# Performance work log

Hardware: AMD Instinct MI355X
Metric: run time of the kernel (lower is better)

Reference implementation:

```python
import jax, jax.numpy as jnp
import numpy as np

TEMPERATURE = 8.0  # sqrt(head_dim=64)
NEG_FILL = -1000000000.0

def setup_inputs() -> dict:
    key = jax.random.key(0)
    k1, k2, k3, k4, k5 = jax.random.split(key, 5)
    B, H, S, D = 4, 16, 1024, 64
    q = jax.random.normal(k1, (B, H, S, D), dtype=jnp.float32)
    k = jax.random.normal(k2, (B, H, S, D), dtype=jnp.float32)
    v = jax.random.normal(k3, (B, H, S, D), dtype=jnp.float32)
    similarity = jax.random.normal(k4, (B, H, S, S), dtype=jnp.float32)
    mask = jax.random.randint(k5, (B, 1, S, S), 0, 2).astype(bool)
    return {"q": q, "k": k, "v": v, "similarity": similarity, "mask": mask}

def reference(q, k, v, similarity, mask):
    # scores: [B,H,S,S] = (q/temp) @ k^T
    attn = jnp.einsum('bhqd,bhkd->bhqk', q / TEMPERATURE, k)
    attn = jnp.where(mask, NEG_FILL, attn)          # masked_fill (mask broadcasts over heads)
    attn = jax.nn.softmax(attn + similarity, axis=-1)  # dropout p=0 (eval): identity
    output = jnp.einsum('bhqk,bhkd->bhqd', attn, v)
    return (output, attn)
```

## Files before the change

kernel.cpp:

```cpp
#include <hip/hip_runtime.h>
#include <stdint.h>


#define S_LEN 1024
#define D_DIM 64
#define QT 16
#define SSTR 1032
#define NEG_FILL (-1000000000.0f)
#define LOG2E 1.44269504088896340736f

typedef __bf16 bf16x8 __attribute__((ext_vector_type(8)));
typedef float f32x4 __attribute__((ext_vector_type(4)));
typedef unsigned short u16x4 __attribute__((ext_vector_type(4)));
typedef unsigned short u16x8 __attribute__((ext_vector_type(8)));

__device__ __forceinline__ unsigned short f2bf(float x) {
    unsigned u = __builtin_bit_cast(unsigned, x);
    u += 0x7fffu + ((u >> 16) & 1u);
    return (unsigned short)(u >> 16);
}
__device__ __forceinline__ float bf2f(unsigned short b) {
    return __builtin_bit_cast(float, (unsigned)b << 16);
}

__global__ void prep_qkm(const float* __restrict__ q, const float* __restrict__ k,
                         const void* __restrict__ mraw,
                         unsigned short* __restrict__ Qb, unsigned short* __restrict__ Kb,
                         unsigned char* __restrict__ Mb)
{
    const int t = threadIdx.x;
    const int i = blockIdx.x * 256 + t;
    f32x4 q4 = ((const f32x4*)q)[i];
    f32x4 k4 = ((const f32x4*)k)[i];
    u16x4 qo, ko;
#pragma unroll
    for (int j = 0; j < 4; ++j) {
        qo[j] = f2bf(q4[j] * 0.125f);
        ko[j] = f2bf(k4[j]);
    }
    ((u16x4*)Qb)[i] = qo;
    ((u16x4*)Kb)[i] = ko;

    __shared__ int s_not_int, s_not_f32;
    if (t == 0) { s_not_int = 0; s_not_f32 = 0; }
    __syncthreads();
    const unsigned* wdd = (const unsigned*)mraw;
    int ni = 0, nf = 0;
    for (int j = t; j < 1024; j += 256) {
        unsigned x = wdd[j];
        if (x > 1u) ni = 1;
        if (x != 0u && x != 0x3f800000u) nf = 1;
    }
    if (ni) s_not_int = 1;
    if (nf) s_not_f32 = 1;
    __syncthreads();
    const int fmt = (s_not_int == 0) ? 0 : ((s_not_f32 == 0) ? 1 : 2);
    uchar4 o;
    if (fmt == 0) {
        int4 x = ((const int4*)mraw)[i];
        o.x = x.x ? 1 : 0; o.y = x.y ? 1 : 0; o.z = x.z ? 1 : 0; o.w = x.w ? 1 : 0;
    } else if (fmt == 1) {
        float4 x = ((const float4*)mraw)[i];
        o.x = (x.x != 0.f) ? 1 : 0; o.y = (x.y != 0.f) ? 1 : 0;
        o.z = (x.z != 0.f) ? 1 : 0; o.w = (x.w != 0.f) ? 1 : 0;
    } else {
        uchar4 x = ((const uchar4*)mraw)[i];
        o.x = x.x ? 1 : 0; o.y = x.y ? 1 : 0; o.z = x.z ? 1 : 0; o.w = x.w ? 1 : 0;
    }
    ((uchar4*)Mb)[i] = o;
}

__global__ void prep_vt(const float* __restrict__ v, unsigned short* __restrict__ Vt)
{
    __shared__ unsigned short sT[64 * 72];
    const int bh = blockIdx.x >> 4;
    const int st = blockIdx.x & 15;
    const int t = threadIdx.x;
    const float* vb = v + (size_t)(bh * S_LEN + st * 64) * D_DIM;
#pragma unroll
    for (int p = 0; p < 4; ++p) {
        int lin = p * 256 + t;
        int r = lin >> 4;
        int c = lin & 15;
        f32x4 x = ((const f32x4*)(vb + r * D_DIM))[c];
        unsigned short* dst = &sT[r * 72 + c * 4];
#pragma unroll
        for (int j = 0; j < 4; ++j) dst[j] = f2bf(x[j]);
    }
    __syncthreads();
    unsigned short* ob = Vt + (size_t)bh * D_DIM * S_LEN + st * 64;
#pragma unroll
    for (int p = 0; p < 4; ++p) {
        int lin = p * 256 + t;
        int d = lin >> 4;
        int s4 = (lin & 15) * 4;
        u16x4 o;
#pragma unroll
        for (int j = 0; j < 4; ++j) o[j] = sT[(s4 + j) * 72 + d];
        *(u16x4*)&ob[d * S_LEN + s4] = o;
    }
}

__global__ __launch_bounds__(256, 4)
void attn_main(const float* __restrict__ simg_, const unsigned short* __restrict__ Qb,
               const unsigned short* __restrict__ Kb, const unsigned short* __restrict__ Vtb,
               const unsigned char* __restrict__ Mb, float* __restrict__ out,
               float* __restrict__ attn)
{
    __shared__ __align__(16) unsigned short sS[QT * SSTR];

    const int blk = blockIdx.x;
    const int bh = blk >> 6;
    const int qt = blk & 63;
    const int b = bh >> 4;
    const int t = threadIdx.x;
    const int w = t >> 6;
    const int lane = t & 63;
    const int quad = lane >> 4;
    const int l15 = lane & 15;

    const unsigned short* Qg = Qb + (size_t)(bh * S_LEN + qt * QT) * D_DIM;
    const unsigned short* Kg = Kb + (size_t)bh * S_LEN * D_DIM;
    const unsigned short* Vg = Vtb + (size_t)bh * D_DIM * S_LEN;
    const float* simg = simg_ + ((size_t)(bh * S_LEN + qt * QT)) * S_LEN;
    const unsigned char* mg = Mb + ((size_t)(b * S_LEN + qt * QT)) * S_LEN;
    float* attng = attn + ((size_t)(bh * S_LEN + qt * QT)) * S_LEN;

    const int n0 = w * 16;
    const bf16x8 av0 = *(const bf16x8*)&Qg[l15 * D_DIM + quad * 8];
    const bf16x8 av1 = *(const bf16x8*)&Qg[l15 * D_DIM + 32 + quad * 8];
#pragma unroll 4
    for (int kt = 0; kt < 16; ++kt) {
        const unsigned short* kp = &Kg[(size_t)(kt * 64 + n0 + l15) * D_DIM + quad * 8];
        bf16x8 bv0 = *(const bf16x8*)kp;
        bf16x8 bv1 = *(const bf16x8*)(kp + 32);
        f32x4 acc = {0.f, 0.f, 0.f, 0.f};
        acc = __builtin_amdgcn_mfma_f32_16x16x32_bf16(av0, bv0, acc, 0, 0, 0);
        acc = __builtin_amdgcn_mfma_f32_16x16x32_bf16(av1, bv1, acc, 0, 0, 0);
        const int colg = kt * 64 + n0 + l15;
#pragma unroll
        for (int r = 0; r < 4; ++r)
            sS[(quad * 4 + r) * SSTR + colg] = f2bf(acc[r]);
    }
    __syncthreads();

#pragma unroll 1
    for (int rr = 0; rr < 4; ++rr) {
        const int row = w * 4 + rr;
        const float* sp = simg + (size_t)row * S_LEN;
        const unsigned char* mp = mg + (size_t)row * S_LEN;
        float vals[16];
        float mx = -3.0e38f;
#pragma unroll
        for (int j = 0; j < 4; ++j) {
            int col = j * 256 + lane * 4;
            u16x4 x = *(const u16x4*)&sS[row * SSTR + col];
            f32x4 sv = *(const f32x4*)&sp[col];
            uchar4 mk = *(const uchar4*)&mp[col];
            float f0 = mk.x ? NEG_FILL : (bf2f(x[0]) + sv[0]);
            float f1 = mk.y ? NEG_FILL : (bf2f(x[1]) + sv[1]);
            float f2 = mk.z ? NEG_FILL : (bf2f(x[2]) + sv[2]);
            float f3 = mk.w ? NEG_FILL : (bf2f(x[3]) + sv[3]);
            vals[j * 4 + 0] = f0; vals[j * 4 + 1] = f1;
            vals[j * 4 + 2] = f2; vals[j * 4 + 3] = f3;
            mx = fmaxf(mx, fmaxf(fmaxf(f0, f1), fmaxf(f2, f3)));
        }
#pragma unroll
        for (int off = 32; off > 0; off >>= 1)
            mx = fmaxf(mx, __shfl_xor(mx, off, 64));
        float sum = 0.f;
#pragma unroll
        for (int i = 0; i < 16; ++i) {
            float e = exp2f((vals[i] - mx) * LOG2E);
            vals[i] = e;
            sum += e;
        }
#pragma unroll
        for (int off = 32; off > 0; off >>= 1)
            sum += __shfl_xor(sum, off, 64);
        const float rinv = 1.0f / sum;
#pragma unroll
        for (int j = 0; j < 4; ++j) {
            int col = j * 256 + lane * 4;
            f32x4 p;
            u16x4 pb;
#pragma unroll
            for (int i = 0; i < 4; ++i) {
                float pi = vals[j * 4 + i] * rinv;
                p[i] = pi;
                pb[i] = f2bf(pi);
            }
            *(f32x4*)&attng[(size_t)row * S_LEN + col] = p;
            *(u16x4*)&sS[row * SSTR + col] = pb;
        }
    }
    __syncthreads();

    f32x4 oacc = {0.f, 0.f, 0.f, 0.f};
    const int d0 = w * 16;
#pragma unroll 4
    for (int kt = 0; kt < 16; ++kt) {
        const unsigned short* vp = &Vg[(size_t)(d0 + l15) * S_LEN + kt * 64 + quad * 8];
        bf16x8 bv0 = *(const bf16x8*)vp;
        bf16x8 bv1 = *(const bf16x8*)(vp + 32);
        bf16x8 pa0 = *(const bf16x8*)&sS[l15 * SSTR + kt * 64 + quad * 8];
        bf16x8 pa1 = *(const bf16x8*)&sS[l15 * SSTR + kt * 64 + 32 + quad * 8];
        oacc = __builtin_amdgcn_mfma_f32_16x16x32_bf16(pa0, bv0, oacc, 0, 0, 0);
        oacc = __builtin_amdgcn_mfma_f32_16x16x32_bf16(pa1, bv1, oacc, 0, 0, 0);
    }
    float* og = out + ((size_t)(bh * S_LEN + qt * QT)) * D_DIM;
#pragma unroll
    for (int r = 0; r < 4; ++r) {
        int row = quad * 4 + r;
        og[row * D_DIM + d0 + l15] = oacc[r];
    }
}

extern "C" void kernel_launch(void* const* d_in, const int* in_sizes, int n_in,
                              void* d_out, int out_size, void* d_ws, size_t ws_size,
                              hipStream_t stream)
{
    const float* q = (const float*)d_in[0];
    const float* k = (const float*)d_in[1];
    const float* v = (const float*)d_in[2];
    const float* sim = (const float*)d_in[3];
    const void* mask = d_in[4];
    float* out = (float*)d_out;
    float* attn = out + (size_t)4 * 16 * 1024 * 64;

    char* ws = (char*)d_ws;
    unsigned short* Qb = (unsigned short*)(ws + (size_t)0);
    unsigned short* Kb = (unsigned short*)(ws + ((size_t)8 << 20));
    unsigned short* Vt = (unsigned short*)(ws + ((size_t)16 << 20));
    unsigned char*  Mb = (unsigned char*)(ws + ((size_t)24 << 20));

    prep_qkm<<<4096, 256, 0, stream>>>(q, k, mask, Qb, Kb, Mb);
    prep_vt<<<1024, 256, 0, stream>>>(v, Vt);
    attn_main<<<4096, 256, 0, stream>>>(sim, Qb, Kb, Vt, Mb, out, attn);
}
```

Before: 574.3 us.

## Prefetch K/V/similarity tiles, XOR-swizzle LDS, nontemporal stores, raise occupancy

```diff
diff --git a/kernel.cpp b/kernel.cpp
--- a/kernel.cpp
+++ b/kernel.cpp
@@ -5,14 +5,12 @@
 #define S_LEN 1024
 #define D_DIM 64
 #define QT 16
-#define SSTR 1032
 #define NEG_FILL (-1000000000.0f)
 #define LOG2E 1.44269504088896340736f
 
 typedef __bf16 bf16x8 __attribute__((ext_vector_type(8)));
 typedef float f32x4 __attribute__((ext_vector_type(4)));
 typedef unsigned short u16x4 __attribute__((ext_vector_type(4)));
-typedef unsigned short u16x8 __attribute__((ext_vector_type(8)));
 
 __device__ __forceinline__ unsigned short f2bf(float x) {
     unsigned u = __builtin_bit_cast(unsigned, x);
@@ -21,6 +19,10 @@
 }
 __device__ __forceinline__ float bf2f(unsigned short b) {
     return __builtin_bit_cast(float, (unsigned)b << 16);
+}
+
+__device__ __forceinline__ unsigned short* sptr(unsigned short* s, int row, int col) {
+    return (unsigned short*)((char*)s + row * 2048 + ((col * 2) ^ ((row & 7) << 4)));
 }
 
 __global__ void prep_qkm(const float* __restrict__ q, const float* __restrict__ k,
@@ -101,13 +103,13 @@
     }
 }
 
-__global__ __launch_bounds__(256, 4)
+__global__ __launch_bounds__(256, 5)
 void attn_main(const float* __restrict__ simg_, const unsigned short* __restrict__ Qb,
                const unsigned short* __restrict__ Kb, const unsigned short* __restrict__ Vtb,
                const unsigned char* __restrict__ Mb, float* __restrict__ out,
                float* __restrict__ attn)
 {
-    __shared__ __align__(16) unsigned short sS[QT * SSTR];
+    __shared__ __align__(16) unsigned short sS[QT * S_LEN];
 
     const int blk = blockIdx.x;
     const int bh = blk >> 6;
@@ -129,34 +131,52 @@
     const int n0 = w * 16;
     const bf16x8 av0 = *(const bf16x8*)&Qg[l15 * D_DIM + quad * 8];
     const bf16x8 av1 = *(const bf16x8*)&Qg[l15 * D_DIM + 32 + quad * 8];
+    const unsigned short* kp0 = &Kg[(size_t)(n0 + l15) * D_DIM + quad * 8];
+    bf16x8 kb0 = *(const bf16x8*)kp0;
+    bf16x8 kb1 = *(const bf16x8*)(kp0 + 32);
 #pragma unroll 4
     for (int kt = 0; kt < 16; ++kt) {
-        const unsigned short* kp = &Kg[(size_t)(kt * 64 + n0 + l15) * D_DIM + quad * 8];
-        bf16x8 bv0 = *(const bf16x8*)kp;
-        bf16x8 bv1 = *(const bf16x8*)(kp + 32);
+        bf16x8 bv0 = kb0, bv1 = kb1;
+        if (kt < 15) {
+            const unsigned short* kp = &Kg[(size_t)((kt + 1) * 64 + n0 + l15) * D_DIM + quad * 8];
+            kb0 = *(const bf16x8*)kp;
+            kb1 = *(const bf16x8*)(kp + 32);
+        }
         f32x4 acc = {0.f, 0.f, 0.f, 0.f};
         acc = __builtin_amdgcn_mfma_f32_16x16x32_bf16(av0, bv0, acc, 0, 0, 0);
         acc = __builtin_amdgcn_mfma_f32_16x16x32_bf16(av1, bv1, acc, 0, 0, 0);
         const int colg = kt * 64 + n0 + l15;
 #pragma unroll
         for (int r = 0; r < 4; ++r)
-            sS[(quad * 4 + r) * SSTR + colg] = f2bf(acc[r]);
-    }
-    __syncthreads();
-
-#pragma unroll 1
+            *sptr(sS, quad * 4 + r, colg) = f2bf(acc[r]);
+    }
+
+    const float* sp_w = simg + (size_t)(w * 4) * S_LEN;
+    f32x4 svb[2][4];
+#pragma unroll
+    for (int j = 0; j < 4; ++j)
+        svb[0][j] = __builtin_nontemporal_load((const f32x4*)&sp_w[j * 256 + lane * 4]);
+    __syncthreads();
+
+#pragma unroll
     for (int rr = 0; rr < 4; ++rr) {
+        const int cb = rr & 1;
         const int row = w * 4 + rr;
-        const float* sp = simg + (size_t)row * S_LEN;
+        if (rr < 3) {
+            const float* spn = sp_w + (size_t)(rr + 1) * S_LEN;
+#pragma unroll
+            for (int j = 0; j < 4; ++j)
+                svb[cb ^ 1][j] = __builtin_nontemporal_load((const f32x4*)&spn[j * 256 + lane * 4]);
+        }
         const unsigned char* mp = mg + (size_t)row * S_LEN;
         float vals[16];
         float mx = -3.0e38f;
 #pragma unroll
         for (int j = 0; j < 4; ++j) {
-            int col = j * 256 + lane * 4;
-            u16x4 x = *(const u16x4*)&sS[row * SSTR + col];
-            f32x4 sv = *(const f32x4*)&sp[col];
+            const int col = j * 256 + lane * 4;
+            u16x4 x = *(const u16x4*)sptr(sS, row, col);
             uchar4 mk = *(const uchar4*)&mp[col];
+            f32x4 sv = svb[cb][j];
             float f0 = mk.x ? NEG_FILL : (bf2f(x[0]) + sv[0]);
             float f1 = mk.y ? NEG_FILL : (bf2f(x[1]) + sv[1]);
             float f2 = mk.z ? NEG_FILL : (bf2f(x[2]) + sv[2]);
@@ -171,7 +191,7 @@
         float sum = 0.f;
 #pragma unroll
         for (int i = 0; i < 16; ++i) {
-            float e = exp2f((vals[i] - mx) * LOG2E);
+            float e = __builtin_amdgcn_exp2f((vals[i] - mx) * LOG2E);
             vals[i] = e;
             sum += e;
         }
@@ -181,7 +201,7 @@
         const float rinv = 1.0f / sum;
 #pragma unroll
         for (int j = 0; j < 4; ++j) {
-            int col = j * 256 + lane * 4;
+            const int col = j * 256 + lane * 4;
             f32x4 p;
             u16x4 pb;
 #pragma unroll
@@ -190,29 +210,36 @@
                 p[i] = pi;
                 pb[i] = f2bf(pi);
             }
-            *(f32x4*)&attng[(size_t)row * S_LEN + col] = p;
-            *(u16x4*)&sS[row * SSTR + col] = pb;
-        }
-    }
+            __builtin_nontemporal_store(p, (f32x4*)&attng[(size_t)row * S_LEN + col]);
+            *(u16x4*)sptr(sS, row, col) = pb;
+        }
+    }
+
+    const int d0 = w * 16;
+    const unsigned short* vpp = &Vg[(size_t)(d0 + l15) * S_LEN + quad * 8];
+    bf16x8 vb0 = *(const bf16x8*)vpp;
+    bf16x8 vb1 = *(const bf16x8*)(vpp + 32);
     __syncthreads();
 
     f32x4 oacc = {0.f, 0.f, 0.f, 0.f};
-    const int d0 = w * 16;
 #pragma unroll 4
     for (int kt = 0; kt < 16; ++kt) {
-        const unsigned short* vp = &Vg[(size_t)(d0 + l15) * S_LEN + kt * 64 + quad * 8];
-        bf16x8 bv0 = *(const bf16x8*)vp;
-        bf16x8 bv1 = *(const bf16x8*)(vp + 32);
-        bf16x8 pa0 = *(const bf16x8*)&sS[l15 * SSTR + kt * 64 + quad * 8];
-        bf16x8 pa1 = *(const bf16x8*)&sS[l15 * SSTR + kt * 64 + 32 + quad * 8];
+        bf16x8 bv0 = vb0, bv1 = vb1;
+        if (kt < 15) {
+            const unsigned short* vp = &Vg[(size_t)(d0 + l15) * S_LEN + (kt + 1) * 64 + quad * 8];
+            vb0 = *(const bf16x8*)vp;
+            vb1 = *(const bf16x8*)(vp + 32);
+        }
+        bf16x8 pa0 = *(const bf16x8*)sptr(sS, l15, kt * 64 + quad * 8);
+        bf16x8 pa1 = *(const bf16x8*)sptr(sS, l15, kt * 64 + 32 + quad * 8);
         oacc = __builtin_amdgcn_mfma_f32_16x16x32_bf16(pa0, bv0, oacc, 0, 0, 0);
         oacc = __builtin_amdgcn_mfma_f32_16x16x32_bf16(pa1, bv1, oacc, 0, 0, 0);
     }
     float* og = out + ((size_t)(bh * S_LEN + qt * QT)) * D_DIM;
 #pragma unroll
     for (int r = 0; r < 4; ++r) {
-        int row = quad * 4 + r;
-        og[row * D_DIM + d0 + l15] = oacc[r];
+        const int row = quad * 4 + r;
+        __builtin_nontemporal_store(oacc[r], &og[row * D_DIM + d0 + l15]);
     }
 }
 
```

Result: no change. 576.9 us (+0.4%).
